# Performance work log

Hardware: AMD Instinct MI355X
Metric: run time of the kernel (lower is better)

## Reference

```python
import jax, jax.numpy as jnp
import numpy as np

N = 100000

def _gcn_layer(x, W, b, src, dst, norm):
    # dense transform then sparse normalized aggregation (scatter-add)
    h = x @ W                                  # [N, out]
    msg = h[src] * norm[:, None]               # [E+N, out]
    agg = jax.ops.segment_sum(msg, dst, num_segments=N)
    return agg + b


def setup_inputs() -> dict:
    key = jax.random.key(0)
    ks = jax.random.split(key, 12)
    num_features, hidden, num_classes = 128, 128, 32
    E = 3200000
    x = jax.random.normal(ks[0], (N, num_features), dtype=jnp.float32)
    edge_index = jax.random.randint(ks[1], (2, E), 0, N, dtype=jnp.int64)

    def glorot(k, fan_in, fan_out):
        s = (6.0 / (fan_in + fan_out)) ** 0.5
        return jax.random.uniform(k, (fan_in, fan_out), jnp.float32, -s, s)

    return {
        "x": x,
        "edge_index": edge_index,
        "W1": glorot(ks[2], num_features, hidden), "b1": jnp.zeros((hidden,), jnp.float32),
        "W2": glorot(ks[3], hidden, hidden),       "b2": jnp.zeros((hidden,), jnp.float32),
        "W3": glorot(ks[4], hidden, hidden),       "b3": jnp.zeros((hidden,), jnp.float32),
        "W4": glorot(ks[5], hidden, num_classes),  "b4": jnp.zeros((num_classes,), jnp.float32),
    }


def reference(x, edge_index, W1, b1, W2, b2, W3, b3, W4, b4):
    # GCNConv semantics: add self-loops, symmetric degree normalization
    loop = jnp.arange(N, dtype=edge_index.dtype)
    src = jnp.concatenate([edge_index[0], loop])   # [E+N]
    dst = jnp.concatenate([edge_index[1], loop])   # [E+N]
    deg = jax.ops.segment_sum(jnp.ones_like(dst, dtype=x.dtype), dst, num_segments=N)
    dinv = jnp.where(deg > 0, deg ** -0.5, 0.0)
    norm = dinv[src] * dinv[dst]                   # [E+N]

    h = _gcn_layer(x, W1, b1, src, dst, norm)
    h = jax.nn.relu(h)                              # dropout: eval mode -> identity
    h = _gcn_layer(h, W2, b2, src, dst, norm)
    h = jax.nn.relu(h)
    h = _gcn_layer(h, W3, b3, src, dst, norm)
    h = jax.nn.relu(h)
    h = _gcn_layer(h, W4, b4, src, dst, norm)
    return jax.nn.log_softmax(h, axis=1)
```

## Files before the change

### kernel.cpp

```cpp
#include <hip/hip_runtime.h>
#include <hip/hip_bf16.h>
#include <math.h>

#define NNODES 100000
#define NBMAX 512
#define CH 8192

typedef __hip_bfloat16 bf16;
typedef __attribute__((ext_vector_type(8))) short short8;
typedef __attribute__((ext_vector_type(4))) float f32x4;
typedef __attribute__((ext_vector_type(2))) float f32x2;

__device__ inline unsigned pack_bf16x2(float a, float b) {
    __hip_bfloat162 p;
    p.x = __float2bfloat16(a);
    p.y = __float2bfloat16(b);
    return *(unsigned*)&p;
}

__device__ inline float2 unpack_bf16x2(unsigned u) {
    __hip_bfloat162 p = *(__hip_bfloat162*)&u;
    return make_float2(__bfloat162float(p.x), __bfloat162float(p.y));
}

__device__ inline unsigned char f32_to_fp8(float v) {
    int p = __builtin_amdgcn_cvt_pk_fp8_f32(v, v, 0, false);
    return (unsigned char)(p & 0xff);
}

__global__ __launch_bounds__(256) void prep_w_all(const float* __restrict__ W1, bf16* __restrict__ wt1,
                                                  const float* __restrict__ W2, bf16* __restrict__ wt2,
                                                  const float* __restrict__ W3, bf16* __restrict__ wt3,
                                                  const float* __restrict__ W4, bf16* __restrict__ wt4,
                                                  int* __restrict__ bcount, int* __restrict__ done,
                                                  unsigned* __restrict__ zrow) {
    int b = blockIdx.x, t = threadIdx.x;
    if (b == 0) {
        for (int i = t; i < NBMAX; i += 256) bcount[i] = 0;
        if (t == 0) *done = 0;
        if (t < 32) zrow[t] = 0u;
    }
    const float* W; bf16* WT; int Nout, idx0;
    if (b < 64)       { W = W1; WT = wt1; Nout = 128; idx0 = b * 256; }
    else if (b < 128) { W = W2; WT = wt2; Nout = 128; idx0 = (b - 64) * 256; }
    else if (b < 192) { W = W3; WT = wt3; Nout = 128; idx0 = (b - 128) * 256; }
    else              { W = W4; WT = wt4; Nout = 32;  idx0 = (b - 192) * 256; }
    int idx = idx0 + t;
    if (idx < 128 * Nout) {
        int nn = idx >> 7;
        int kk = idx & 127;
        WT[idx] = __float2bfloat16(W[kk * Nout + nn]);
    }
}

__global__ __launch_bounds__(256) void bucket_hist_scan(const int* __restrict__ dst,
                                                        int* __restrict__ bcount,
                                                        int* __restrict__ boff,
                                                        int* __restrict__ bcursor,
                                                        int* __restrict__ off,
                                                        int* __restrict__ done,
                                                        int E, int nb, int n, int nblocks) {
    __shared__ int hist[NBMAX];
    __shared__ int ticket_s;
    __shared__ int wsum[4];
    int t = threadIdx.x;
    for (int i = t; i < NBMAX; i += 256) hist[i] = 0;
    __syncthreads();
    int e0 = blockIdx.x * CH;
#pragma unroll
    for (int k = 0; k < 32; ++k) {
        int e = e0 + t + k * 256;
        if (e < E) atomicAdd(&hist[dst[e] >> 8], 1);
    }
    __syncthreads();
    for (int i = t; i < nb; i += 256)
        if (hist[i]) atomicAdd(&bcount[i], hist[i]);
    __threadfence();
    __syncthreads();
    if (t == 0) ticket_s = atomicAdd(done, 1);
    __syncthreads();
    if (ticket_s != nblocks - 1) return;
    __threadfence();
    int i0 = t * 2, i1v = t * 2 + 1;
    int a  = (i0  < nb) ? atomicAdd(&bcount[i0], 0) : 0;
    int bb = (i1v < nb) ? atomicAdd(&bcount[i1v], 0) : 0;
    int v = a + bb;
    int lane = t & 63, wv = t >> 6;
    int incl = v;
#pragma unroll
    for (int dd = 1; dd < 64; dd <<= 1) {
        int x = __shfl_up(incl, dd, 64);
        if (lane >= dd) incl += x;
    }
    if (lane == 63) wsum[wv] = incl;
    __syncthreads();
    int wo = 0;
    for (int k = 0; k < wv; ++k) wo += wsum[k];
    int excl = wo + incl - v;
    if (i0 <= nb)  { boff[i0]  = excl;     if (i0  < nb) bcursor[i0]  = excl; }
    if (i1v <= nb) { boff[i1v] = excl + a; if (i1v < nb) bcursor[i1v] = excl + a; }
    if (t == 255) off[n] = excl + v;
}

__global__ __launch_bounds__(256) void partition(const int* __restrict__ src,
                                                 const int* __restrict__ dst,
                                                 int* __restrict__ bcursor,
                                                 int2* __restrict__ part, int E, int nb) {
    __shared__ int hist[NBMAX];
    __shared__ int lstart[NBMAX];
    __shared__ int gbase[NBMAX];
    __shared__ int cursor[NBMAX];
    __shared__ int2 sorted[CH];
    int t = threadIdx.x;
    int e0 = blockIdx.x * CH;
    for (int i = t; i < NBMAX; i += 256) hist[i] = 0;
    __syncthreads();
    int mys[32], myd[32];
#pragma unroll
    for (int k = 0; k < 32; ++k) {
        int e = e0 + t + k * 256;
        int s = 0, d = -1;
        if (e < E) { s = src[e]; d = dst[e]; }
        mys[k] = s; myd[k] = d;
        if (d >= 0) atomicAdd(&hist[d >> 8], 1);
    }
    __syncthreads();
    if (t < 64) {
        int base = t * 8;
        int tmp[8];
        int sum = 0;
#pragma unroll
        for (int j = 0; j < 8; ++j) { tmp[j] = hist[base + j]; sum += tmp[j]; }
        int incl = sum;
#pragma unroll
        for (int d = 1; d < 64; d <<= 1) {
            int x = __shfl_up(incl, d, 64);
            if (t >= d) incl += x;
        }
        int excl = incl - sum;
#pragma unroll
        for (int j = 0; j < 8; ++j) {
            lstart[base + j] = excl;
            cursor[base + j] = excl;
            excl += tmp[j];
        }
    }
    __syncthreads();
    for (int i = t; i < nb; i += 256) {
        int c = hist[i];
        gbase[i] = c ? atomicAdd(&bcursor[i], c) : 0;
    }
    __syncthreads();
#pragma unroll
    for (int k = 0; k < 32; ++k) {
        int d = myd[k];
        if (d >= 0) {
            int lpos = atomicAdd(&cursor[d >> 8], 1);
            sorted[lpos] = make_int2(mys[k], d);
        }
    }
    __syncthreads();
    int cnt = min(CH, E - e0);
    for (int i = t; i < cnt; i += 256) {
        int2 rec = sorted[i];
        int b = rec.y >> 8;
        part[gbase[b] + (i - lstart[b])] = rec;
    }
}

__global__ __launch_bounds__(256) void nodes_fill(const int2* __restrict__ part,
                                                  const int* __restrict__ boff,
                                                  float* __restrict__ dinv,
                                                  int* __restrict__ off,
                                                  int* __restrict__ edges, int n) {
    __shared__ int ndeg[256];
    __shared__ int ws2[4];
    __shared__ int offl[256];
    int b = blockIdx.x;
    int t = threadIdx.x;
    ndeg[t] = 0;
    __syncthreads();
    int r0 = boff[b], r1 = boff[b + 1];
    for (int i = r0 + t; i < r1; i += 256)
        atomicAdd(&ndeg[part[i].y & 255], 1);
    __syncthreads();
    int deg = ndeg[t];
    int node = b * 256 + t;
    int lane = t & 63, wv = t >> 6;
    int incl = deg;
#pragma unroll
    for (int d = 1; d < 64; d <<= 1) {
        int x = __shfl_up(incl, d, 64);
        if (lane >= d) incl += x;
    }
    if (lane == 63) ws2[wv] = incl;
    __syncthreads();
    int wo = 0;
    for (int k = 0; k < wv; ++k) wo += ws2[k];
    int node_off = r0 + wo + incl - deg;
    if (node < n) {
        off[node] = node_off;
        dinv[node] = rsqrtf((float)(deg + 1));
    }
    offl[t] = node_off;
    ndeg[t] = 0;
    __syncthreads();
    for (int i = r0 + t; i < r1; i += 256) {
        int2 rec = part[i];
        int dloc = rec.y & 255;
        int lpos = atomicAdd(&ndeg[dloc], 1);
        edges[offl[dloc] + lpos] = rec.x;
    }
}

#define WSTRIDE 136

__global__ __launch_bounds__(256) void gemm128_f32A(const float* __restrict__ A,
                                                    const bf16* __restrict__ WT,
                                                    const float* __restrict__ dinv,
                                                    unsigned char* __restrict__ C, int n) {
    __shared__ bf16 wl[128 * WSTRIDE];
    int t = threadIdx.x;
#pragma unroll
    for (int l = 0; l < 8; ++l) {
        int chunk = t + l * 256;
        int row = chunk >> 4, ch = chunk & 15;
        *(uint4*)&wl[row * WSTRIDE + ch * 8] = *(const uint4*)&WT[row * 128 + ch * 8];
    }
    __syncthreads();
    int wave = t >> 6, lane = t & 63;
    int m = lane & 15, q = lane >> 4;
    int row_base = blockIdx.x * 128 + wave * 32;
    int r0 = min(row_base + m, n - 1);
    int r1 = min(row_base + 16 + m, n - 1);

    f32x4 acc[2][8];
#pragma unroll
    for (int g = 0; g < 2; ++g)
#pragma unroll
        for (int c = 0; c < 8; ++c) acc[g][c] = (f32x4)(0.f);

#pragma unroll
    for (int kt = 0; kt < 4; ++kt) {
        short8 af[2];
#pragma unroll
        for (int g = 0; g < 2; ++g) {
            const float* ap = &A[(size_t)(g ? r1 : r0) * 128 + kt * 32 + q * 8];
            float4 f0 = *(const float4*)ap;
            float4 f1 = *(const float4*)(ap + 4);
            union { uint4 u; short8 s; } cv;
            cv.u.x = pack_bf16x2(f0.x, f0.y);
            cv.u.y = pack_bf16x2(f0.z, f0.w);
            cv.u.z = pack_bf16x2(f1.x, f1.y);
            cv.u.w = pack_bf16x2(f1.z, f1.w);
            af[g] = cv.s;
        }
#pragma unroll
        for (int c = 0; c < 8; ++c) {
            short8 bf = *(const short8*)&wl[(c * 16 + m) * WSTRIDE + kt * 32 + q * 8];
            acc[0][c] = __builtin_amdgcn_mfma_f32_16x16x32_bf16(af[0], bf, acc[0][c], 0, 0, 0);
            acc[1][c] = __builtin_amdgcn_mfma_f32_16x16x32_bf16(af[1], bf, acc[1][c], 0, 0, 0);
        }
    }
    float dv[2][4];
#pragma unroll
    for (int g = 0; g < 2; ++g)
#pragma unroll
        for (int r = 0; r < 4; ++r) {
            int row = row_base + g * 16 + q * 4 + r;
            dv[g][r] = (row < n) ? dinv[row] : 0.f;
        }
#pragma unroll
    for (int g = 0; g < 2; ++g)
#pragma unroll
        for (int c = 0; c < 8; ++c)
#pragma unroll
            for (int r = 0; r < 4; ++r) {
                int row = row_base + g * 16 + q * 4 + r;
                if (row < n) C[(size_t)row * 128 + c * 16 + m] = f32_to_fp8(acc[g][c][r] * dv[g][r]);
            }
}

__global__ __launch_bounds__(256) void gemm128_bf16A(const bf16* __restrict__ A,
                                                     const bf16* __restrict__ WT,
                                                     const float* __restrict__ dinv,
                                                     unsigned char* __restrict__ C, int n) {
    __shared__ bf16 wl[128 * WSTRIDE];
    int t = threadIdx.x;
#pragma unroll
    for (int l = 0; l < 8; ++l) {
        int chunk = t + l * 256;
        int row = chunk >> 4, ch = chunk & 15;
        *(uint4*)&wl[row * WSTRIDE + ch * 8] = *(const uint4*)&WT[row * 128 + ch * 8];
    }
    __syncthreads();
    int wave = t >> 6, lane = t & 63;
    int m = lane & 15, q = lane >> 4;
    int row_base = blockIdx.x * 128 + wave * 32;
    int r0 = min(row_base + m, n - 1);
    int r1 = min(row_base + 16 + m, n - 1);

    f32x4 acc[2][8];
#pragma unroll
    for (int g = 0; g < 2; ++g)
#pragma unroll
        for (int c = 0; c < 8; ++c) acc[g][c] = (f32x4)(0.f);

#pragma unroll
    for (int kt = 0; kt < 4; ++kt) {
        short8 a0 = *(const short8*)&A[(size_t)r0 * 128 + kt * 32 + q * 8];
        short8 a1 = *(const short8*)&A[(size_t)r1 * 128 + kt * 32 + q * 8];
#pragma unroll
        for (int c = 0; c < 8; ++c) {
            short8 bf = *(const short8*)&wl[(c * 16 + m) * WSTRIDE + kt * 32 + q * 8];
            acc[0][c] = __builtin_amdgcn_mfma_f32_16x16x32_bf16(a0, bf, acc[0][c], 0, 0, 0);
            acc[1][c] = __builtin_amdgcn_mfma_f32_16x16x32_bf16(a1, bf, acc[1][c], 0, 0, 0);
        }
    }
    float dv[2][4];
#pragma unroll
    for (int g = 0; g < 2; ++g)
#pragma unroll
        for (int r = 0; r < 4; ++r) {
            int row = row_base + g * 16 + q * 4 + r;
            dv[g][r] = (row < n) ? dinv[row] : 0.f;
        }
#pragma unroll
    for (int g = 0; g < 2; ++g)
#pragma unroll
        for (int c = 0; c < 8; ++c)
#pragma unroll
            for (int r = 0; r < 4; ++r) {
                int row = row_base + g * 16 + q * 4 + r;
                if (row < n) C[(size_t)row * 128 + c * 16 + m] = f32_to_fp8(acc[g][c][r] * dv[g][r]);
            }
}

__global__ __launch_bounds__(256) void gemm32_bf16A(const bf16* __restrict__ A,
                                                    const bf16* __restrict__ WT,
                                                    const float* __restrict__ dinv,
                                                    bf16* __restrict__ C, int n) {
    if (blockIdx.x == 0 && threadIdx.x < 32)
        C[(size_t)n * 32 + threadIdx.x] = __float2bfloat16(0.f);
    int wave = threadIdx.x >> 6;
    int lane = threadIdx.x & 63;
    int m = lane & 15;
    int q = lane >> 4;
    int row_base = blockIdx.x * 64 + wave * 16;
    int arow = min(row_base + m, n - 1);

    f32x4 acc[2];
    acc[0] = (f32x4)(0.f);
    acc[1] = (f32x4)(0.f);

#pragma unroll
    for (int kt = 0; kt < 4; ++kt) {
        short8 af = *(const short8*)&A[(size_t)arow * 128 + kt * 32 + q * 8];
#pragma unroll
        for (int c = 0; c < 2; ++c) {
            short8 bf = *(const short8*)&WT[(size_t)(c * 16 + m) * 128 + kt * 32 + q * 8];
            acc[c] = __builtin_amdgcn_mfma_f32_16x16x32_bf16(af, bf, acc[c], 0, 0, 0);
        }
    }
    float dv[4];
#pragma unroll
    for (int r = 0; r < 4; ++r) {
        int row = row_base + q * 4 + r;
        dv[r] = (row < n) ? dinv[row] : 0.f;
    }
#pragma unroll
    for (int c = 0; c < 2; ++c)
#pragma unroll
        for (int r = 0; r < 4; ++r) {
            int row = row_base + q * 4 + r;
            if (row < n) C[(size_t)row * 32 + c * 16 + m] = __float2bfloat16(acc[c][r] * dv[r]);
        }
}

__global__ __launch_bounds__(256) void agg128(const unsigned char* __restrict__ h,
                                              const int* __restrict__ off,
                                              const int* __restrict__ edges,
                                              const float* __restrict__ dinv,
                                              const float* __restrict__ bias,
                                              bf16* __restrict__ out, int n) {
    int wid = (blockIdx.x * blockDim.x + threadIdx.x) >> 6;
    if (wid >= n) return;
    int lane = threadIdx.x & 63;
    int g = lane >> 4;
    int d = lane & 15;
    const char* hb = (const char*)h;
    unsigned doff = (unsigned)(d << 3);

    f32x2 A0 = {0.f, 0.f}, A1 = {0.f, 0.f}, A2 = {0.f, 0.f}, A3 = {0.f, 0.f};
    {
        uint2 su = *(const uint2*)(hb + (((unsigned)wid << 7) | doff));
        if (g) { su.x = 0u; su.y = 0u; }
        A0 += __builtin_amdgcn_cvt_pk_f32_fp8((int)su.x, false);
        A1 += __builtin_amdgcn_cvt_pk_f32_fp8((int)su.x, true);
        A2 += __builtin_amdgcn_cvt_pk_f32_fp8((int)su.y, false);
        A3 += __builtin_amdgcn_cvt_pk_f32_fp8((int)su.y, true);
    }

    int i0 = off[wid], i1 = off[wid + 1];
    int i = i0;
    while (i1 - i > 64) {
        int id2[16];
#pragma unroll
        for (int j = 0; j < 16; ++j) id2[j] = edges[i + j * 4 + g];
        uint2 uu[16];
#pragma unroll
        for (int j = 0; j < 16; ++j)
            uu[j] = *(const uint2*)(hb + (((unsigned)id2[j] << 7) | doff));
#pragma unroll
        for (int j = 0; j < 16; ++j) {
            A0 += __builtin_amdgcn_cvt_pk_f32_fp8((int)uu[j].x, false);
            A1 += __builtin_amdgcn_cvt_pk_f32_fp8((int)uu[j].x, true);
            A2 += __builtin_amdgcn_cvt_pk_f32_fp8((int)uu[j].y, false);
            A3 += __builtin_amdgcn_cvt_pk_f32_fp8((int)uu[j].y, true);
        }
        i += 64;
    }
    {
        int rem = i1 - i;
        int nj = (rem + 3) >> 2;
        int id2[16];
        uint2 uu[16];
#pragma unroll
        for (int j = 0; j < 16; ++j) {
            if (j < nj) {
                int e = i + j * 4 + g;
                int s = edges[e];
                if (e >= i1) s = n;
                id2[j] = s;
            }
        }
#pragma unroll
        for (int j = 0; j < 16; ++j)
            if (j < nj) uu[j] = *(const uint2*)(hb + (((unsigned)id2[j] << 7) | doff));
#pragma unroll
        for (int j = 0; j < 16; ++j) {
            if (j < nj) {
                A0 += __builtin_amdgcn_cvt_pk_f32_fp8((int)uu[j].x, false);
                A1 += __builtin_amdgcn_cvt_pk_f32_fp8((int)uu[j].x, true);
                A2 += __builtin_amdgcn_cvt_pk_f32_fp8((int)uu[j].y, false);
                A3 += __builtin_amdgcn_cvt_pk_f32_fp8((int)uu[j].y, true);
            }
        }
    }
    float r0 = A0[0], r1 = A0[1], r2 = A1[0], r3 = A1[1];
    float r4 = A2[0], r5 = A2[1], r6 = A3[0], r7 = A3[1];
    r0 += __shfl_xor(r0, 16); r1 += __shfl_xor(r1, 16);
    r2 += __shfl_xor(r2, 16); r3 += __shfl_xor(r3, 16);
    r4 += __shfl_xor(r4, 16); r5 += __shfl_xor(r5, 16);
    r6 += __shfl_xor(r6, 16); r7 += __shfl_xor(r7, 16);
    r0 += __shfl_xor(r0, 32); r1 += __shfl_xor(r1, 32);
    r2 += __shfl_xor(r2, 32); r3 += __shfl_xor(r3, 32);
    r4 += __shfl_xor(r4, 32); r5 += __shfl_xor(r5, 32);
    r6 += __shfl_xor(r6, 32); r7 += __shfl_xor(r7, 32);
    float pa = (g & 1) ? r2 : r0;
    float pb = (g & 1) ? r3 : r1;
    float qa = (g & 1) ? r6 : r4;
    float qb = (g & 1) ? r7 : r5;
    pa = (g & 2) ? qa : pa;
    pb = (g & 2) ? qb : pb;

    float dl = dinv[wid];
    int od = d * 4 + g;
    float2 bv = *(const float2*)&bias[od * 2];
    float a0 = fmaxf(pa * dl + bv.x, 0.f);
    float a1 = fmaxf(pb * dl + bv.y, 0.f);
    ((unsigned*)out)[(size_t)wid * 64 + od] = pack_bf16x2(a0, a1);
}

__global__ __launch_bounds__(256) void agg32_lsm(const bf16* __restrict__ h,
                                                 const int* __restrict__ off,
                                                 const int* __restrict__ edges,
                                                 const float* __restrict__ dinv,
                                                 const float* __restrict__ bias,
                                                 float* __restrict__ out, int n) {
    int idx = blockIdx.x * blockDim.x + threadIdx.x;
    int node = idx >> 5;
    if (node >= n) return;
    int lane5 = idx & 31;
    int g = lane5 >> 3;
    int d = lane5 & 7;
    const char* hb = (const char*)h;
    unsigned doff = (unsigned)(d << 3);

    f32x2 acc0 = {0.f, 0.f}, acc1 = {0.f, 0.f};
    {
        uint2 su = *(const uint2*)(hb + (((unsigned)node << 6) | doff));
        if (g) { su.x = 0u; su.y = 0u; }
        float2 f0 = unpack_bf16x2(su.x), f1 = unpack_bf16x2(su.y);
        acc0[0] += f0.x; acc0[1] += f0.y; acc1[0] += f1.x; acc1[1] += f1.y;
    }
    int i0 = off[node], i1 = off[node + 1];
    int i = i0;
    while (i1 - i > 64) {
        int id2[16];
#pragma unroll
        for (int j = 0; j < 16; ++j) id2[j] = edges[i + j * 4 + g];
        uint2 uu[16];
#pragma unroll
        for (int j = 0; j < 16; ++j)
            uu[j] = *(const uint2*)(hb + (((unsigned)id2[j] << 6) | doff));
#pragma unroll
        for (int j = 0; j < 16; ++j) {
            float2 f0 = unpack_bf16x2(uu[j].x), f1 = unpack_bf16x2(uu[j].y);
            acc0[0] += f0.x; acc0[1] += f0.y; acc1[0] += f1.x; acc1[1] += f1.y;
        }
        i += 64;
    }
    {
        int rem = i1 - i;
        int nj = (rem + 3) >> 2;
        int id2[16];
        uint2 uu[16];
#pragma unroll
        for (int j = 0; j < 16; ++j) {
            if (j < nj) {
                int e = i + j * 4 + g;
                int s = edges[e];
                if (e >= i1) s = n;
                id2[j] = s;
            }
        }
#pragma unroll
        for (int j = 0; j < 16; ++j)
            if (j < nj) uu[j] = *(const uint2*)(hb + (((unsigned)id2[j] << 6) | doff));
#pragma unroll
        for (int j = 0; j < 16; ++j) {
            if (j < nj) {
                float2 f0 = unpack_bf16x2(uu[j].x), f1 = unpack_bf16x2(uu[j].y);
                acc0[0] += f0.x; acc0[1] += f0.y; acc1[0] += f1.x; acc1[1] += f1.y;
            }
        }
    }
    float s0 = acc0[0], s1 = acc0[1], s2 = acc1[0], s3 = acc1[1];
    s0 += __shfl_xor(s0, 8);  s1 += __shfl_xor(s1, 8);
    s2 += __shfl_xor(s2, 8);  s3 += __shfl_xor(s3, 8);
    s0 += __shfl_xor(s0, 16); s1 += __shfl_xor(s1, 16);
    s2 += __shfl_xor(s2, 16); s3 += __shfl_xor(s3, 16);

    float dl = dinv[node];
    float4 bv = *(const float4*)&bias[d * 4];
    float a0 = s0 * dl + bv.x;
    float a1 = s1 * dl + bv.y;
    float a2 = s2 * dl + bv.z;
    float a3 = s3 * dl + bv.w;
    float m = fmaxf(fmaxf(a0, a1), fmaxf(a2, a3));
    for (int dd = 1; dd < 8; dd <<= 1) m = fmaxf(m, __shfl_xor(m, dd));
    float e = expf(a0 - m) + expf(a1 - m) + expf(a2 - m) + expf(a3 - m);
    for (int dd = 1; dd < 8; dd <<= 1) e += __shfl_xor(e, dd);
    float lse = m + logf(e);
    if (g == 0)
        *(float4*)&out[(size_t)node * 32 + d * 4] =
            make_float4(a0 - lse, a1 - lse, a2 - lse, a3 - lse);
}

extern "C" void kernel_launch(void* const* d_in, const int* in_sizes, int n_in,
                              void* d_out, int out_size, void* d_ws, size_t ws_size,
                              hipStream_t stream) {
    const float* x  = (const float*)d_in[0];
    const int*   ei = (const int*)d_in[1];
    const float* W1 = (const float*)d_in[2];
    const float* b1 = (const float*)d_in[3];
    const float* W2 = (const float*)d_in[4];
    const float* b2 = (const float*)d_in[5];
    const float* W3 = (const float*)d_in[6];
    const float* b3 = (const float*)d_in[7];
    const float* W4 = (const float*)d_in[8];
    const float* b4 = (const float*)d_in[9];
    float* out = (float*)d_out;

    const int N = NNODES;
    const int E = in_sizes[1] / 2;
    const int nb = (N + 255) / 256;

    char* ws = (char*)d_ws;
    size_t o = 0;
    auto alloc = [&](size_t bytes) -> void* {
        void* p = ws + o;
        o += (bytes + 255) & ~(size_t)255;
        return p;
    };
    int*   bcount  = (int*)alloc((size_t)NBMAX * 4);
    int*   boff    = (int*)alloc((size_t)(NBMAX + 1) * 4);
    int*   bcursor = (int*)alloc((size_t)NBMAX * 4);
    int*   done    = (int*)alloc(4);
    int*   off     = (int*)alloc((size_t)(N + 1) * 4);
    float* dinv    = (float*)alloc((size_t)N * 4);
    int2*  part    = (int2*)alloc((size_t)E * 8);
    int*   edges   = (int*)alloc((size_t)(E + 64) * 4);
    bf16*  wt1     = (bf16*)alloc((size_t)128 * 128 * 2);
    bf16*  wt2     = (bf16*)alloc((size_t)128 * 128 * 2);
    bf16*  wt3     = (bf16*)alloc((size_t)128 * 128 * 2);
    bf16*  wt4     = (bf16*)alloc((size_t)32 * 128 * 2);
    unsigned char* hbuf = (unsigned char*)alloc((size_t)(N + 1) * 128);
    bf16*  gbuf    = (bf16*)part;

    const int* srcv = ei;
    const int* dstv = ei + E;

    int pblocks = (E + CH - 1) / CH;

    prep_w_all<<<208, 256, 0, stream>>>(W1, wt1, W2, wt2, W3, wt3, W4, wt4,
                                        bcount, done, (unsigned*)(hbuf + (size_t)N * 128));
    bucket_hist_scan<<<pblocks, 256, 0, stream>>>(dstv, bcount, boff, bcursor, off, done,
                                                  E, nb, N, pblocks);
    partition<<<pblocks, 256, 0, stream>>>(srcv, dstv, bcursor, part, E, nb);
    nodes_fill<<<nb, 256, 0, stream>>>(part, boff, dinv, off, edges, N);

    int gemm128_blocks = (N + 127) / 128;
    int gemm32_blocks = (N + 63) / 64;
    int agg128_blocks = (N + 3) / 4;
    int agg32_blocks = (N * 32 + 255) / 256;

    gemm128_f32A<<<gemm128_blocks, 256, 0, stream>>>(x, wt1, dinv, hbuf, N);
    agg128<<<agg128_blocks, 256, 0, stream>>>(hbuf, off, edges, dinv, b1, gbuf, N);
    gemm128_bf16A<<<gemm128_blocks, 256, 0, stream>>>(gbuf, wt2, dinv, hbuf, N);
    agg128<<<agg128_blocks, 256, 0, stream>>>(hbuf, off, edges, dinv, b2, gbuf, N);
    gemm128_bf16A<<<gemm128_blocks, 256, 0, stream>>>(gbuf, wt3, dinv, hbuf, N);
    agg128<<<agg128_blocks, 256, 0, stream>>>(hbuf, off, edges, dinv, b3, gbuf, N);
    gemm32_bf16A<<<gemm32_blocks, 256, 0, stream>>>(gbuf, wt4, dinv, (bf16*)hbuf, N);
    agg32_lsm<<<agg32_blocks, 256, 0, stream>>>((const bf16*)hbuf, off, edges, dinv, b4, out, N);
}
```

Measured before the change: 536.4 us.

## Pack partition records into one int and software-pipeline gather index loads

The partition kernel now writes each edge as a single 32-bit word (source in the low 24 bits, local destination in the high 8 bits) straight to global memory, dropping the shared-memory sort stage and halving partition traffic. nodes_fill decodes the packed word. The fp8 and bf16 gather loops use smaller batches (8 or 4 index groups), prefetch the next batch of indices while the current rows are loaded, and preload the tail indices up front. The trade-off is less coalesced scattered global writes in partition, a 24-bit limit on source ids, and less memory-level parallelism per iteration in the gather loops.

```diff
diff --git a/kernel.cpp b/kernel.cpp
--- a/kernel.cpp
+++ b/kernel.cpp
@@ -105,12 +105,9 @@
 __global__ __launch_bounds__(256) void partition(const int* __restrict__ src,
                                                  const int* __restrict__ dst,
                                                  int* __restrict__ bcursor,
-                                                 int2* __restrict__ part, int E, int nb) {
+                                                 int* __restrict__ part, int E, int nb) {
     __shared__ int hist[NBMAX];
-    __shared__ int lstart[NBMAX];
-    __shared__ int gbase[NBMAX];
     __shared__ int cursor[NBMAX];
-    __shared__ int2 sorted[CH];
     int t = threadIdx.x;
     int e0 = blockIdx.x * CH;
     for (int i = t; i < NBMAX; i += 256) hist[i] = 0;
@@ -119,56 +116,28 @@
 #pragma unroll
     for (int k = 0; k < 32; ++k) {
         int e = e0 + t + k * 256;
-        int s = 0, d = -1;
-        if (e < E) { s = src[e]; d = dst[e]; }
-        mys[k] = s; myd[k] = d;
-        if (d >= 0) atomicAdd(&hist[d >> 8], 1);
-    }
-    __syncthreads();
-    if (t < 64) {
-        int base = t * 8;
-        int tmp[8];
-        int sum = 0;
-#pragma unroll
-        for (int j = 0; j < 8; ++j) { tmp[j] = hist[base + j]; sum += tmp[j]; }
-        int incl = sum;
-#pragma unroll
-        for (int d = 1; d < 64; d <<= 1) {
-            int x = __shfl_up(incl, d, 64);
-            if (t >= d) incl += x;
-        }
-        int excl = incl - sum;
-#pragma unroll
-        for (int j = 0; j < 8; ++j) {
-            lstart[base + j] = excl;
-            cursor[base + j] = excl;
-            excl += tmp[j];
-        }
+        int s = 0, dd = -1;
+        if (e < E) { s = src[e]; dd = dst[e]; }
+        mys[k] = s; myd[k] = dd;
+        if (dd >= 0) atomicAdd(&hist[dd >> 8], 1);
     }
     __syncthreads();
     for (int i = t; i < nb; i += 256) {
         int c = hist[i];
-        gbase[i] = c ? atomicAdd(&bcursor[i], c) : 0;
+        cursor[i] = c ? atomicAdd(&bcursor[i], c) : 0;
     }
     __syncthreads();
 #pragma unroll
     for (int k = 0; k < 32; ++k) {
-        int d = myd[k];
-        if (d >= 0) {
-            int lpos = atomicAdd(&cursor[d >> 8], 1);
-            sorted[lpos] = make_int2(mys[k], d);
-        }
-    }
-    __syncthreads();
-    int cnt = min(CH, E - e0);
-    for (int i = t; i < cnt; i += 256) {
-        int2 rec = sorted[i];
-        int b = rec.y >> 8;
-        part[gbase[b] + (i - lstart[b])] = rec;
-    }
-}
-
-__global__ __launch_bounds__(256) void nodes_fill(const int2* __restrict__ part,
+        int dd = myd[k];
+        if (dd >= 0) {
+            int lpos = atomicAdd(&cursor[dd >> 8], 1);
+            part[lpos] = mys[k] | ((dd & 255) << 24);
+        }
+    }
+}
+
+__global__ __launch_bounds__(256) void nodes_fill(const int* __restrict__ part,
                                                   const int* __restrict__ boff,
                                                   float* __restrict__ dinv,
                                                   int* __restrict__ off,
@@ -182,7 +151,7 @@
     __syncthreads();
     int r0 = boff[b], r1 = boff[b + 1];
     for (int i = r0 + t; i < r1; i += 256)
-        atomicAdd(&ndeg[part[i].y & 255], 1);
+        atomicAdd(&ndeg[((unsigned)part[i]) >> 24], 1);
     __syncthreads();
     int deg = ndeg[t];
     int node = b * 256 + t;
@@ -206,10 +175,10 @@
     ndeg[t] = 0;
     __syncthreads();
     for (int i = r0 + t; i < r1; i += 256) {
-        int2 rec = part[i];
-        int dloc = rec.y & 255;
+        int rec = part[i];
+        int dloc = ((unsigned)rec) >> 24;
         int lpos = atomicAdd(&ndeg[dloc], 1);
-        edges[offl[dloc] + lpos] = rec.x;
+        edges[offl[dloc] + lpos] = rec & 0xFFFFFF;
     }
 }
 
@@ -402,43 +371,51 @@
     }
 
     int i0 = off[wid], i1 = off[wid + 1];
+    int deg = i1 - i0;
+    int tail = i0 + (deg & ~31);
+    int nj = (i1 - tail + 3) >> 2;
+    int idt[8];
+#pragma unroll
+    for (int j = 0; j < 8; ++j) {
+        if (j < nj) {
+            int e = tail + j * 4 + g;
+            int s = edges[e];
+            if (e >= i1) s = n;
+            idt[j] = s;
+        }
+    }
     int i = i0;
-    while (i1 - i > 64) {
-        int id2[16];
-#pragma unroll
-        for (int j = 0; j < 16; ++j) id2[j] = edges[i + j * 4 + g];
-        uint2 uu[16];
-#pragma unroll
-        for (int j = 0; j < 16; ++j)
-            uu[j] = *(const uint2*)(hb + (((unsigned)id2[j] << 7) | doff));
-#pragma unroll
-        for (int j = 0; j < 16; ++j) {
+    int id[8];
+    if (i + 32 <= i1) {
+#pragma unroll
+        for (int j = 0; j < 8; ++j) id[j] = edges[i + j * 4 + g];
+    }
+    while (i + 32 <= i1) {
+        uint2 uu[8];
+#pragma unroll
+        for (int j = 0; j < 8; ++j)
+            uu[j] = *(const uint2*)(hb + (((unsigned)id[j] << 7) | doff));
+        int inext = i + 32;
+        if (inext + 32 <= i1) {
+#pragma unroll
+            for (int j = 0; j < 8; ++j) id[j] = edges[inext + j * 4 + g];
+        }
+#pragma unroll
+        for (int j = 0; j < 8; ++j) {
             A0 += __builtin_amdgcn_cvt_pk_f32_fp8((int)uu[j].x, false);
             A1 += __builtin_amdgcn_cvt_pk_f32_fp8((int)uu[j].x, true);
             A2 += __builtin_amdgcn_cvt_pk_f32_fp8((int)uu[j].y, false);
             A3 += __builtin_amdgcn_cvt_pk_f32_fp8((int)uu[j].y, true);
         }
-        i += 64;
+        i = inext;
     }
     {
-        int rem = i1 - i;
-        int nj = (rem + 3) >> 2;
-        int id2[16];
-        uint2 uu[16];
-#pragma unroll
-        for (int j = 0; j < 16; ++j) {
-            if (j < nj) {
-                int e = i + j * 4 + g;
-                int s = edges[e];
-                if (e >= i1) s = n;
-                id2[j] = s;
-            }
-        }
-#pragma unroll
-        for (int j = 0; j < 16; ++j)
-            if (j < nj) uu[j] = *(const uint2*)(hb + (((unsigned)id2[j] << 7) | doff));
-#pragma unroll
-        for (int j = 0; j < 16; ++j) {
+        uint2 uu[8];
+#pragma unroll
+        for (int j = 0; j < 8; ++j)
+            if (j < nj) uu[j] = *(const uint2*)(hb + (((unsigned)idt[j] << 7) | doff));
+#pragma unroll
+        for (int j = 0; j < 8; ++j) {
             if (j < nj) {
                 A0 += __builtin_amdgcn_cvt_pk_f32_fp8((int)uu[j].x, false);
                 A1 += __builtin_amdgcn_cvt_pk_f32_fp8((int)uu[j].x, true);
@@ -495,41 +472,49 @@
         acc0[0] += f0.x; acc0[1] += f0.y; acc1[0] += f1.x; acc1[1] += f1.y;
     }
     int i0 = off[node], i1 = off[node + 1];
+    int deg = i1 - i0;
+    int tail = i0 + (deg & ~15);
+    int nj = (i1 - tail + 3) >> 2;
+    int idt[4];
+#pragma unroll
+    for (int j = 0; j < 4; ++j) {
+        if (j < nj) {
+            int e = tail + j * 4 + g;
+            int s = edges[e];
+            if (e >= i1) s = n;
+            idt[j] = s;
+        }
+    }
     int i = i0;
-    while (i1 - i > 64) {
-        int id2[16];
-#pragma unroll
-        for (int j = 0; j < 16; ++j) id2[j] = edges[i + j * 4 + g];
-        uint2 uu[16];
-#pragma unroll
-        for (int j = 0; j < 16; ++j)
-            uu[j] = *(const uint2*)(hb + (((unsigned)id2[j] << 6) | doff));
-#pragma unroll
-        for (int j = 0; j < 16; ++j) {
+    int id[4];
+    if (i + 16 <= i1) {
+#pragma unroll
+        for (int j = 0; j < 4; ++j) id[j] = edges[i + j * 4 + g];
+    }
+    while (i + 16 <= i1) {
+        uint2 uu[4];
+#pragma unroll
+        for (int j = 0; j < 4; ++j)
+            uu[j] = *(const uint2*)(hb + (((unsigned)id[j] << 6) | doff));
+        int inext = i + 16;
+        if (inext + 16 <= i1) {
+#pragma unroll
+            for (int j = 0; j < 4; ++j) id[j] = edges[inext + j * 4 + g];
+        }
+#pragma unroll
+        for (int j = 0; j < 4; ++j) {
             float2 f0 = unpack_bf16x2(uu[j].x), f1 = unpack_bf16x2(uu[j].y);
             acc0[0] += f0.x; acc0[1] += f0.y; acc1[0] += f1.x; acc1[1] += f1.y;
         }
-        i += 64;
+        i = inext;
     }
     {
-        int rem = i1 - i;
-        int nj = (rem + 3) >> 2;
-        int id2[16];
-        uint2 uu[16];
-#pragma unroll
-        for (int j = 0; j < 16; ++j) {
-            if (j < nj) {
-                int e = i + j * 4 + g;
-                int s = edges[e];
-                if (e >= i1) s = n;
-                id2[j] = s;
-            }
-        }
-#pragma unroll
-        for (int j = 0; j < 16; ++j)
-            if (j < nj) uu[j] = *(const uint2*)(hb + (((unsigned)id2[j] << 6) | doff));
-#pragma unroll
-        for (int j = 0; j < 16; ++j) {
+        uint2 uu[4];
+#pragma unroll
+        for (int j = 0; j < 4; ++j)
+            if (j < nj) uu[j] = *(const uint2*)(hb + (((unsigned)idt[j] << 6) | doff));
+#pragma unroll
+        for (int j = 0; j < 4; ++j) {
             if (j < nj) {
                 float2 f0 = unpack_bf16x2(uu[j].x), f1 = unpack_bf16x2(uu[j].y);
                 acc0[0] += f0.x; acc0[1] += f0.y; acc1[0] += f1.x; acc1[1] += f1.y;
@@ -590,7 +575,7 @@
     int*   done    = (int*)alloc(4);
     int*   off     = (int*)alloc((size_t)(N + 1) * 4);
     float* dinv    = (float*)alloc((size_t)N * 4);
-    int2*  part    = (int2*)alloc((size_t)E * 8);
+    int*   part    = (int*)alloc((size_t)E * 8);
     int*   edges   = (int*)alloc((size_t)(E + 64) * 4);
     bf16*  wt1     = (bf16*)alloc((size_t)128 * 128 * 2);
     bf16*  wt2     = (bf16*)alloc((size_t)128 * 128 * 2);
```

Result: faster. 495.2 us (-7.7%).
